# Optimization experiments

Hardware: AMD Instinct MI355X
Metric: run time of the kernel (lower is better)

The kernel has to match this reference:

```python
import jax, jax.numpy as jnp
import numpy as np

KSIZE = 21
PAD = (KSIZE - 1) // 2
SCALE = 4
W0, W1, W2 = 1.0, 1.0, 1.0  # cfg.SOLVER.SR_LOSS_FUNC_SR_WEIGHT


def setup_inputs() -> dict:
    key = jax.random.key(0)
    ks = jax.random.split(key, 7)
    B, C, H, W = 16, 3, 512, 512
    return {
        "hr_pred": jax.random.normal(ks[0], (B, C, H, W), jnp.float32),
        "hr_target": jax.random.normal(ks[1], (B, C, H, W), jnp.float32),
        "lr_target": jax.random.normal(ks[2], (B, C, H // SCALE, W // SCALE), jnp.float32),
        "kernel_pred": jax.random.uniform(ks[3], (B, KSIZE * KSIZE, 64, 64), jnp.float32),
        "gt_kernel": jax.random.uniform(ks[4], (B, 1, KSIZE, KSIZE), jnp.float32),
        "segment_preds": jax.random.uniform(ks[5], (B, 1, H, W), jnp.float32),
        "segment_targets": jax.random.uniform(ks[6], (B, 1, H, W), jnp.float32),
        "iter": 1000,
    }


def _per_sample_blur(img, ker):
    # img: [C,H,W], ker: [k,k] -> depthwise conv with the same kernel on each channel
    C = img.shape[0]
    w = jnp.broadcast_to(ker[None, None], (C, 1, KSIZE, KSIZE))
    out = jax.lax.conv_general_dilated(
        img[None], w, window_strides=(1, 1),
        padding=[(PAD, PAD), (PAD, PAD)], feature_group_count=C)
    return out[0]


def _get_pseudo_lr(sr, kernel_feat):
    # GAP over spatial dims, normalize over channel dim -> per-sample blur kernel
    k = kernel_feat.mean(axis=(2, 3))                      # [B, k*k]
    k = k / k.sum(axis=1, keepdims=True)
    weight = k.reshape(k.shape[0], 1, KSIZE, KSIZE)        # [B,1,k,k]
    blurred = jax.vmap(_per_sample_blur)(sr, weight[:, 0])  # [B,C,H,W]
    B, C, H, W = blurred.shape
    lrs = jax.image.resize(blurred, (B, C, H // SCALE, W // SCALE), method="bicubic")
    return lrs, weight


def reference(hr_pred, hr_target, lr_target, kernel_pred, gt_kernel,
              segment_preds, segment_targets, iter):
    hr_loss = jnp.abs(hr_pred - hr_target)                 # L1, reduction='none'
    lr_pred, kernel_w = _get_pseudo_lr(hr_pred, kernel_pred)
    lr_loss = jnp.abs(lr_pred - lr_target)
    kernel_loss = jnp.square(kernel_w - gt_kernel)         # MSE, reduction='none'
    # ORIENTED_WEIGHT_ITER == -1 -> no crack/seg-fail weighting
    # ONLY_KERNEL_LOSS_FOR_PRETRAIN == False -> full weighted sum
    loss = (W0 * hr_loss.mean(axis=(1, 2, 3))
            + W1 * lr_loss.mean(axis=(1, 2, 3))
            + W2 * kernel_loss.mean(axis=(1, 2, 3)))       # [B]
    return loss, kernel_w
```

## Files before the change

kernel.cpp:

```cpp
#include <hip/hip_runtime.h>

#define NB 16
#define NC 3
#define NH 512
#define NW 512
#define TAPS 441
#define HL 128
#define WL 128

#define WS_KSUM   0
#define WS_WEIGHT 7056
#define WS_FCLASS 14112
#define WS_FPOLY  532512
#define WS_KLMEAN 560160
#define WS_HRPART 560176
#define WS_LRPOLY 561200
#define WS_LREDGE 561968
#define WS_TOTAL  574064
#define WS_LRB    574064
#define WS_W4     577000
#define WS_FPOLY2 3722728
#define WS_TOTAL3 3745256
#define WS_HRP2   3745256
#define WS_TOTAL4 3748328

__device__ inline float keysCubic(float x) {
  if (x < 1.f) return ((1.5f * x - 2.5f) * x) * x + 1.f;
  if (x < 2.f) return ((-0.5f * x + 2.5f) * x - 4.f) * x + 2.f;
  return 0.f;
}

__device__ inline float blockSumAll(float v, volatile float* red, int nw) {
  #pragma unroll
  for (int o = 32; o > 0; o >>= 1) v += __shfl_down(v, o, 64);
  int w = threadIdx.x >> 6, lane = threadIdx.x & 63;
  __syncthreads();
  if (lane == 0) red[w] = v;
  __syncthreads();
  float s = 0.f;
  for (int i = 0; i < nw; i++) s += red[i];
  return s;
}

__global__ void zero_accum(float* p, int n) {
  int t = blockIdx.x * blockDim.x + threadIdx.x;
  if (t < n) p[t] = 0.f;
}

__global__ void kmean_kernel(const float4* __restrict__ kp4, float* __restrict__ ksum) {
  __shared__ float red[4];
  int blk = blockIdx.x;
  int t = threadIdx.x;
  const float4* base = kp4 + (size_t)blk * 1024;
  float s = 0.f;
  #pragma unroll
  for (int i = 0; i < 4; i++) {
    float4 v = base[i * 256 + t];
    s += v.x + v.y + v.z + v.w;
  }
  float tot = blockSumAll(s, red, 4);
  if (t == 0) ksum[blk] = tot * (1.f / 4096.f);
}

__global__ void knorm_kernel(const float* __restrict__ ksum, const float* __restrict__ gt,
                             float* __restrict__ weight, float* __restrict__ kw_out,
                             float* __restrict__ kl_mean) {
  __shared__ float red[8];
  int b = blockIdx.x, t = threadIdx.x;
  float v = (t < TAPS) ? ksum[b * TAPS + t] : 0.f;
  float tot = blockSumAll(v, red, 8);
  float sq = 0.f;
  if (t < TAPS) {
    float w = v / tot;
    weight[b * TAPS + t] = w;
    kw_out[b * TAPS + t] = w;
    float d = w - gt[b * TAPS + t];
    sq = d * d;
  }
  float sqs = blockSumAll(sq, red, 8);
  if (t == 0) kl_mean[b] = sqs * (1.f / (float)TAPS);
}

__global__ void hrloss_kernel(const float4* __restrict__ a, const float4* __restrict__ bb,
                              float* __restrict__ hr_part) {
  __shared__ float red[4];
  int blk = blockIdx.x, t = threadIdx.x;
  int samp = blk >> 6, chunk = blk & 63;
  size_t base = (size_t)samp * 196608 + (size_t)chunk * 3072;
  float s = 0.f;
  #pragma unroll
  for (int i = 0; i < 12; i++) {
    float4 x = a[base + i * 256 + t];
    float4 y = bb[base + i * 256 + t];
    s += fabsf(x.x - y.x) + fabsf(x.y - y.y) + fabsf(x.z - y.z) + fabsf(x.w - y.w);
  }
  float tot = blockSumAll(s, red, 4);
  if (t == 0) hr_part[blk] = tot;
}

__global__ void precls_kernel(const float* __restrict__ ws_weight, float* __restrict__ fclass,
                              float* __restrict__ fpoly, float* __restrict__ fpoly2) {
  __shared__ float ker[441];
  __shared__ float H[21][36];
  __shared__ float Qy[16], Qx[16];
  int cy = blockIdx.x / 5, cx = blockIdx.x % 5, b = blockIdx.y;
  int t = threadIdx.x;
  for (int i = t; i < 441; i += 256) ker[i] = ws_weight[b * 441 + i];
  if (t == 0) {
    const int lo[5] = {6, 2, 0, 0, 0};
    const int hi[5] = {16, 16, 16, 14, 10};
    float s = 0.f;
    for (int k = 0; k < 16; k++) {
      float q = (k >= lo[cy] && k < hi[cy]) ? keysCubic(fabsf((float)k - 7.5f) * 0.25f) : 0.f;
      Qy[k] = q; s += q;
    }
    for (int k = 0; k < 16; k++) Qy[k] /= s;
    s = 0.f;
    for (int k = 0; k < 16; k++) {
      float q = (k >= lo[cx] && k < hi[cx]) ? keysCubic(fabsf((float)k - 7.5f) * 0.25f) : 0.f;
      Qx[k] = q; s += q;
    }
    for (int k = 0; k < 16; k++) Qx[k] /= s;
  }
  bool interior = (cy == 2 && cx == 2);
  if (interior) {
    for (int i = t; i < 1728; i += 256) fpoly[b * 1728 + i] = 0.f;
  }
  __syncthreads();
  for (int i = t; i < 756; i += 256) {
    int ty = i / 36, q = i - (i / 36) * 36;
    float s = 0.f;
    int tx0 = max(0, q - 15), tx1 = min(21, q + 1);
    for (int tx = tx0; tx < tx1; tx++) s += ker[ty * 21 + tx] * Qx[q - tx];
    H[ty][q] = s;
  }
  __syncthreads();
  float* Fb = fclass + ((size_t)b * 25 + (size_t)blockIdx.x) * 1296;
  for (int i = t; i < 1296; i += 256) {
    int p = i / 36, q = i - (i / 36) * 36;
    float s = 0.f;
    int ty0 = max(0, p - 15), ty1 = min(21, p + 1);
    for (int ty = ty0; ty < ty1; ty++) s += Qy[p - ty] * H[ty][q];
    Fb[i] = s;
    if (interior) {
      int phase = (p & 3) * 4 + (q & 3);
      fpoly[b * 1728 + phase * 108 + (p >> 2) * 12 + (q >> 2)] = s;
      if (fpoly2)
        fpoly2[b * 1408 + phase * 88 + (p >> 2) * 9 + (q >> 2)] = s;
    }
  }
}

__global__ __launch_bounds__(256, 5) void conv_phase4f(const float* __restrict__ img,
                                                       const float* __restrict__ tgt,
                                                       const float* __restrict__ fpoly2,
                                                       float* __restrict__ W4,
                                                       float* __restrict__ hrp) {
  __shared__ __align__(16) float SM[7040];
  __shared__ float redh[4];
  int z = blockIdx.z;
  int bc = z >> 2, phy = z & 3;
  int b = bc / 3;
  int tileX = blockIdx.x, tileY = blockIdx.y;
  int t = threadIdx.x;
  int phx = t >> 6;
  int pos = t & 63;
  int gy_ = pos >> 3;
  int gx_ = pos & 7;

  int rowBase = 128 * tileY - 16 + phy;
  int colBase = 128 * tileX - 16;
  const float* imgbc = img + (size_t)bc * (NH * NW);
  const float* tgtbc = tgt + (size_t)bc * (NH * NW);
  float l1 = 0.f;
  for (int idx = t; idx < 1600; idx += 256) {
    int yy = idx / 40, xx = idx - (idx / 40) * 40;
    int gy = rowBase + 4 * yy;
    int gx = colBase + 4 * xx;
    float4 v = {0.f, 0.f, 0.f, 0.f};
    if ((unsigned)gy < (unsigned)NH && (unsigned)gx < (unsigned)NW)
      v = *(const float4*)&imgbc[(size_t)gy * NW + gx];
    SM[0 * 1760 + yy * 44 + xx] = v.x;
    SM[1 * 1760 + yy * 44 + xx] = v.y;
    SM[2 * 1760 + yy * 44 + xx] = v.z;
    SM[3 * 1760 + yy * 44 + xx] = v.w;
    if (yy >= 4 && yy < 36 && xx >= 4 && xx < 36) {
      float4 tv = *(const float4*)&tgtbc[(size_t)gy * NW + gx];
      l1 += fabsf(v.x - tv.x) + fabsf(v.y - tv.y) + fabsf(v.z - tv.z) + fabsf(v.w - tv.w);
    }
  }
  __syncthreads();
  float hsum = blockSumAll(l1, redh, 4);
  if (t == 0) hrp[(blockIdx.z * 4 + blockIdx.y) * 4 + blockIdx.x] = hsum;

  float acc[4][4];
  #pragma unroll
  for (int r = 0; r < 4; r++)
    #pragma unroll
    for (int j = 0; j < 4; j++) acc[r][j] = 0.f;

  int foff = __builtin_amdgcn_readfirstlane(b * 1408 + (phy * 4 + phx) * 88);
  const float* fk = fpoly2 + foff;
  int smbase = __builtin_amdgcn_readfirstlane(phx * 1760);
  const float* Sp = &SM[smbase];
  #pragma unroll
  for (int m = 0; m < 12; m++) {
    const float* srow = &Sp[(4 * gy_ + m) * 44 + 4 * gx_];
    float4 a0 = *(const float4*)srow;
    float4 a1 = *(const float4*)(srow + 4);
    float4 a2 = *(const float4*)(srow + 8);
    float rowv[12] = {a0.x, a0.y, a0.z, a0.w, a1.x, a1.y, a1.z, a1.w,
                      a2.x, a2.y, a2.z, a2.w};
    #pragma unroll
    for (int r = 0; r < 4; r++) {
      int uy = m - r;
      if (uy >= 0 && uy < 9) {
        #pragma unroll
        for (int q = 0; q < 9; q++) {
          float fv = fk[uy * 9 + q];
          #pragma unroll
          for (int j = 0; j < 4; j++)
            acc[r][j] = fmaf(fv, rowv[q + j], acc[r][j]);
        }
      }
    }
  }

  __syncthreads();
  #pragma unroll
  for (int r = 0; r < 4; r++) {
    float4 s = {acc[r][0], acc[r][1], acc[r][2], acc[r][3]};
    *(float4*)&SM[phx * 1024 + (4 * gy_ + r) * 32 + 4 * gx_] = s;
  }
  __syncthreads();

  const float4* R0 = (const float4*)&SM[0];
  const float4* R1 = (const float4*)&SM[1024];
  const float4* R2 = (const float4*)&SM[2048];
  const float4* R3 = (const float4*)&SM[3072];
  float4 v0 = R0[t], v1 = R1[t], v2 = R2[t], v3 = R3[t];
  float4 s;
  s.x = v0.x + v1.x + v2.x + v3.x;
  s.y = v0.y + v1.y + v2.y + v3.y;
  s.z = v0.z + v1.z + v2.z + v3.z;
  s.w = v0.w + v1.w + v2.w + v3.w;

  int oy = 32 * tileY + (t >> 3);
  int ox = 32 * tileX + 4 * (t & 7);
  float* dst = W4 + ((size_t)phy * 48 + bc) * (HL * WL) + (size_t)oy * WL + ox;
  *(float4*)dst = s;
}

__global__ __launch_bounds__(256) void lrsum_kernel(const float* __restrict__ W4,
                                                    const float* __restrict__ lr_tgt,
                                                    float* __restrict__ lr_b) {
  __shared__ float red[4];
  int bc = blockIdx.y;
  int idx = blockIdx.x * 256 + threadIdx.x;
  float l = 0.f;
  if (idx < 15376) {
    int oy = 2 + idx / 124;
    int ox = 2 + (idx - (idx / 124) * 124);
    size_t base = (size_t)bc * (HL * WL) + (size_t)oy * WL + ox;
    const size_t PL = (size_t)48 * HL * WL;
    float s = W4[base] + W4[base + PL] + W4[base + 2 * PL] + W4[base + 3 * PL];
    l = fabsf(s - lr_tgt[base]);
  }
  float tot = blockSumAll(l, red, 4);
  if (threadIdx.x == 0) lr_b[bc * 61 + blockIdx.x] = tot;
}

__global__ __launch_bounds__(128) void fused_poly(const float* __restrict__ img,
                                                  const float* __restrict__ lr_tgt,
                                                  const float4* __restrict__ fpoly4,
                                                  float* __restrict__ lr_poly) {
  __shared__ __align__(16) float S[4][40][44];
  __shared__ float red[2];
  int tileX = blockIdx.x, tileY = blockIdx.y, bc = blockIdx.z;
  int b = bc / 3;
  int t = threadIdx.x;
  int oyT = t >> 2, oxG = t & 3;
  const float* imgbc = img + (size_t)bc * (NH * NW);
  const float4* fp4 = fpoly4 + b * 432;
  float acc[8] = {0.f, 0.f, 0.f, 0.f, 0.f, 0.f, 0.f, 0.f};
  int rowBase = 128 * tileY - 16;
  int colBase = 128 * tileX - 16;
  for (int phy = 0; phy < 4; phy++) {
    for (int idx = t; idx < 1600; idx += 128) {
      int yy = idx / 40, xx = idx - yy * 40;
      int gy = rowBase + 4 * yy + phy;
      int gx = colBase + 4 * xx;
      float4 v = {0.f, 0.f, 0.f, 0.f};
      if ((unsigned)gy < (unsigned)NH && (unsigned)gx < (unsigned)NW)
        v = *(const float4*)&imgbc[(size_t)gy * NW + gx];
      S[0][yy][xx] = v.x; S[1][yy][xx] = v.y; S[2][yy][xx] = v.z; S[3][yy][xx] = v.w;
    }
    __syncthreads();
    #pragma unroll
    for (int phx = 0; phx < 4; phx++) {
      const float4* fprow = fp4 + (phy * 4 + phx) * 27;
      for (int uy = 0; uy < 9; uy++) {
        const float* srow = &S[phx][oyT + uy][oxG * 8];
        float4 w0 = *(const float4*)(srow);
        float4 w1 = *(const float4*)(srow + 4);
        float4 w2 = *(const float4*)(srow + 8);
        float4 w3 = *(const float4*)(srow + 12);
        float w[16] = {w0.x, w0.y, w0.z, w0.w, w1.x, w1.y, w1.z, w1.w,
                       w2.x, w2.y, w2.z, w2.w, w3.x, w3.y, w3.z, w3.w};
        float4 f0 = fprow[uy * 3], f1 = fprow[uy * 3 + 1], f2 = fprow[uy * 3 + 2];
        float f[9] = {f0.x, f0.y, f0.z, f0.w, f1.x, f1.y, f1.z, f1.w, f2.x};
        #pragma unroll
        for (int q = 0; q < 9; q++) {
          #pragma unroll
          for (int r = 0; r < 8; r++) acc[r] = fmaf(f[q], w[q + r], acc[r]);
        }
      }
    }
    __syncthreads();
  }
  int oy = 32 * tileY + oyT;
  float l = 0.f;
  if (oy >= 2 && oy < 126) {
    const float* tg = lr_tgt + (size_t)bc * (HL * WL) + (size_t)oy * WL + 32 * tileX + oxG * 8;
    #pragma unroll
    for (int r = 0; r < 8; r++) {
      int ox = 32 * tileX + oxG * 8 + r;
      if (ox >= 2 && ox < 126) l += fabsf(acc[r] - tg[r]);
    }
  }
  float tot = blockSumAll(l, red, 2);
  if (t == 0) lr_poly[bc * 16 + tileY * 4 + tileX] = tot;
}

__global__ __launch_bounds__(256) void edge_kernel(const float* __restrict__ img,
                                                   const float* __restrict__ lr_tgt,
                                                   const float* __restrict__ fclass,
                                                   float* __restrict__ lr_edge) {
  __shared__ float red[4];
  int bc = blockIdx.y, b = bc / 3;
  int wid = threadIdx.x >> 6, lane = threadIdx.x & 63;
  int idx = blockIdx.x * 4 + wid;
  int oy, ox;
  if (idx < 512) {
    int e = idx >> 7;
    oy = (e < 2) ? e : (124 + e);
    ox = idx & 127;
  } else {
    int j = idx - 512;
    oy = 2 + (j >> 2);
    int c = j & 3;
    ox = (c < 2) ? c : (124 + c);
  }
  int cy = (oy == 0) ? 0 : (oy == 1) ? 1 : (oy == 126) ? 3 : (oy == 127) ? 4 : 2;
  int cx = (ox == 0) ? 0 : (ox == 1) ? 1 : (ox == 126) ? 3 : (ox == 127) ? 4 : 2;
  const float* F = fclass + ((size_t)b * 25 + (size_t)(cy * 5 + cx)) * 1296;
  const float* imgbc = img + (size_t)bc * (NH * NW);
  int gy0 = 4 * oy - 16, gx0 = 4 * ox - 16;
  float acc = 0.f;
  #pragma unroll 3
  for (int tp = lane; tp < 1296; tp += 64) {
    int p = (unsigned)tp / 36u;
    int q = tp - p * 36;
    int gy = gy0 + p, gx = gx0 + q;
    float v = 0.f;
    if ((unsigned)gy < (unsigned)NH && (unsigned)gx < (unsigned)NW)
      v = imgbc[gy * NW + gx];
    acc = fmaf(F[tp], v, acc);
  }
  #pragma unroll
  for (int o = 32; o > 0; o >>= 1) acc += __shfl_down(acc, o, 64);
  __syncthreads();
  if (lane == 0) {
    float tgt = lr_tgt[(size_t)bc * (HL * WL) + (size_t)oy * WL + ox];
    red[wid] = fabsf(acc - tgt);
  }
  __syncthreads();
  if (threadIdx.x == 0) {
    lr_edge[bc * 252 + blockIdx.x] = red[0] + red[1] + red[2] + red[3];
  }
}

__global__ void final_big4(const float* __restrict__ hrp, const float* __restrict__ lr_b,
                           const float* __restrict__ lr_edge, const float* __restrict__ kl_mean,
                           float* __restrict__ out) {
  __shared__ float red[4];
  int b = blockIdx.x, t = threadIdx.x;
  float hs = 0.f;
  for (int i = t; i < 192; i += 256) hs += hrp[b * 192 + i];
  float h = blockSumAll(hs, red, 4);
  float ls = 0.f;
  for (int i = t; i < 183; i += 256) ls += lr_b[b * 183 + i];
  for (int i = t; i < 756; i += 256) ls += lr_edge[b * 756 + i];
  float l = blockSumAll(ls, red, 4);
  if (t == 0)
    out[b] = h * (1.f / 786432.f) + l * (1.f / 49152.f) + kl_mean[b];
}

__global__ void final_reduce(const float* __restrict__ hr_part, const float* __restrict__ lr_poly,
                             const float* __restrict__ lr_edge, const float* __restrict__ kl_mean,
                             float* __restrict__ out) {
  __shared__ float red[4];
  int b = blockIdx.x, t = threadIdx.x;
  float hs = 0.f;
  for (int i = t; i < 64; i += 256) hs += hr_part[b * 64 + i];
  float h = blockSumAll(hs, red, 4);
  float ls = 0.f;
  for (int i = t; i < 48; i += 256) ls += lr_poly[b * 48 + i];
  for (int i = t; i < 756; i += 256) ls += lr_edge[b * 756 + i];
  float l = blockSumAll(ls, red, 4);
  if (t == 0)
    out[b] = h * (1.f / 786432.f) + l * (1.f / 49152.f) + kl_mean[b];
}

extern "C" void kernel_launch(void* const* d_in, const int* in_sizes, int n_in,
                              void* d_out, int out_size, void* d_ws, size_t ws_size,
                              hipStream_t stream) {
  const float* hr_pred = (const float*)d_in[0];
  const float* hr_target = (const float*)d_in[1];
  const float* lr_target = (const float*)d_in[2];
  const float* kernel_pred = (const float*)d_in[3];
  const float* gt_kernel = (const float*)d_in[4];
  float* out = (float*)d_out;
  float* ws = (float*)d_ws;

  bool big4 = ws_size >= (size_t)WS_TOTAL4 * sizeof(float);
  bool big = ws_size >= (size_t)WS_TOTAL * sizeof(float);
  float* ksum = ws + WS_KSUM;
  float* weight = ws + WS_WEIGHT;

  if (big) {
    float* fclass = ws + WS_FCLASS;
    float* fpoly = ws + WS_FPOLY;
    float* kl_mean = ws + WS_KLMEAN;
    float* lr_edge = ws + WS_LREDGE;
    float* fpoly2 = big4 ? (ws + WS_FPOLY2) : nullptr;
    kmean_kernel<<<NB * TAPS, 256, 0, stream>>>((const float4*)kernel_pred, ksum);
    knorm_kernel<<<NB, 512, 0, stream>>>(ksum, gt_kernel, weight, out + NB, kl_mean);
    precls_kernel<<<dim3(25, NB), 256, 0, stream>>>(weight, fclass, fpoly, fpoly2);
    edge_kernel<<<dim3(252, NB * NC), 256, 0, stream>>>(hr_pred, lr_target, fclass, lr_edge);
    if (big4) {
      float* lr_b = ws + WS_LRB;
      float* W4 = ws + WS_W4;
      float* hrp = ws + WS_HRP2;
      conv_phase4f<<<dim3(4, 4, NB * NC * 4), 256, 0, stream>>>(hr_pred, hr_target, fpoly2,
                                                                W4, hrp);
      lrsum_kernel<<<dim3(61, NB * NC), 256, 0, stream>>>(W4, lr_target, lr_b);
      final_big4<<<NB, 256, 0, stream>>>(hrp, lr_b, lr_edge, kl_mean, out);
    } else {
      float* hr_part = ws + WS_HRPART;
      float* lr_poly = ws + WS_LRPOLY;
      hrloss_kernel<<<NB * 64, 256, 0, stream>>>((const float4*)hr_pred,
                                                 (const float4*)hr_target, hr_part);
      fused_poly<<<dim3(4, 4, NB * NC), 128, 0, stream>>>(hr_pred, lr_target,
                                                          (const float4*)fpoly, lr_poly);
      final_reduce<<<NB, 256, 0, stream>>>(hr_part, lr_poly, lr_edge, kl_mean, out);
    }
  } else {
    float* hr_sum = ws + 14112;
    float* lr_sum = hr_sum + 16;
    float* kl_mean = hr_sum + 32;
    zero_accum<<<1, 64, 0, stream>>>(hr_sum, 48);
    kmean_kernel<<<NB * TAPS, 256, 0, stream>>>((const float4*)kernel_pred, ksum);
    knorm_kernel<<<NB, 512, 0, stream>>>(ksum, gt_kernel, weight, out + NB, kl_mean);
    hrloss_kernel<<<NB * 64, 256, 0, stream>>>((const float4*)hr_pred, (const float4*)hr_target,
                                               ksum);
    final_reduce<<<NB, 256, 0, stream>>>(ksum, lr_sum, lr_sum, kl_mean, out);
  }
}
```

Measured before the change: 124.1 us.

## Merge edge-pixel kernel into main conv kernel via interleaved block ranges

Folds the separate edge_kernel launch into the phase-conv kernel. A 1D grid of 79*192 blocks is split so each group of 79 runs 16 interior conv blocks and 63 border-pixel blocks. This removes one launch and the serialization between the edge and conv stages, so the light edge work can overlap with the heavy conv blocks. In exchange, the merged kernel carries the larger launch bounds and shared memory footprint for the edge blocks, and blockIdx is decoded by hand.

After: 128.2 us. +3.4%, slower.

```diff
diff --git a/kernel.cpp b/kernel.cpp
--- a/kernel.cpp
+++ b/kernel.cpp
@@ -20,7 +20,6 @@
 #define WS_LRB    574064
 #define WS_W4     577000
 #define WS_FPOLY2 3722728
-#define WS_TOTAL3 3745256
 #define WS_HRP2   3745256
 #define WS_TOTAL4 3748328
 
@@ -151,18 +150,70 @@
   }
 }
 
-__global__ __launch_bounds__(256, 5) void conv_phase4f(const float* __restrict__ img,
-                                                       const float* __restrict__ tgt,
-                                                       const float* __restrict__ fpoly2,
-                                                       float* __restrict__ W4,
-                                                       float* __restrict__ hrp) {
+__global__ __launch_bounds__(256, 5) void main_fused(const float* __restrict__ img,
+                                                     const float* __restrict__ tgt,
+                                                     const float* __restrict__ lr_tgt,
+                                                     const float* __restrict__ fpoly2,
+                                                     const float* __restrict__ fclass,
+                                                     float* __restrict__ W4,
+                                                     float* __restrict__ hrp,
+                                                     float* __restrict__ lr_edge) {
   __shared__ __align__(16) float SM[7040];
   __shared__ float redh[4];
-  int z = blockIdx.z;
+  int bid = blockIdx.x;
+  int g = bid / 79, r = bid - g * 79;
+  int t = threadIdx.x;
+
+  if (r >= 16) {
+    int eb = g * 63 + (r - 16);
+    int bc = eb / 252, xblk = eb - bc * 252;
+    int b = bc / 3;
+    int wid = t >> 6, lane = t & 63;
+    int idx = xblk * 4 + wid;
+    int oy, ox;
+    if (idx < 512) {
+      int e = idx >> 7;
+      oy = (e < 2) ? e : (124 + e);
+      ox = idx & 127;
+    } else {
+      int j = idx - 512;
+      oy = 2 + (j >> 2);
+      int c = j & 3;
+      ox = (c < 2) ? c : (124 + c);
+    }
+    int cy = (oy == 0) ? 0 : (oy == 1) ? 1 : (oy == 126) ? 3 : (oy == 127) ? 4 : 2;
+    int cx = (ox == 0) ? 0 : (ox == 1) ? 1 : (ox == 126) ? 3 : (ox == 127) ? 4 : 2;
+    const float* F = fclass + ((size_t)b * 25 + (size_t)(cy * 5 + cx)) * 1296;
+    const float* imgbc = img + (size_t)bc * (NH * NW);
+    int gy0 = 4 * oy - 16, gx0 = 4 * ox - 16;
+    float acc = 0.f;
+    #pragma unroll 3
+    for (int tp = lane; tp < 1296; tp += 64) {
+      int p = (unsigned)tp / 36u;
+      int q = tp - p * 36;
+      int gy = gy0 + p, gx = gx0 + q;
+      float v = 0.f;
+      if ((unsigned)gy < (unsigned)NH && (unsigned)gx < (unsigned)NW)
+        v = imgbc[gy * NW + gx];
+      acc = fmaf(F[tp], v, acc);
+    }
+    #pragma unroll
+    for (int o = 32; o > 0; o >>= 1) acc += __shfl_down(acc, o, 64);
+    __syncthreads();
+    if (lane == 0) {
+      float tv = lr_tgt[(size_t)bc * (HL * WL) + (size_t)oy * WL + ox];
+      redh[wid] = fabsf(acc - tv);
+    }
+    __syncthreads();
+    if (t == 0)
+      lr_edge[bc * 252 + xblk] = redh[0] + redh[1] + redh[2] + redh[3];
+    return;
+  }
+
+  int cb = g * 16 + r;
+  int tileX = cb & 3, tileY = (cb >> 2) & 3, z = cb >> 4;
   int bc = z >> 2, phy = z & 3;
   int b = bc / 3;
-  int tileX = blockIdx.x, tileY = blockIdx.y;
-  int t = threadIdx.x;
   int phx = t >> 6;
   int pos = t & 63;
   int gy_ = pos >> 3;
@@ -191,13 +242,13 @@
   }
   __syncthreads();
   float hsum = blockSumAll(l1, redh, 4);
-  if (t == 0) hrp[(blockIdx.z * 4 + blockIdx.y) * 4 + blockIdx.x] = hsum;
+  if (t == 0) hrp[(z * 4 + tileY) * 4 + tileX] = hsum;
 
   float acc[4][4];
   #pragma unroll
-  for (int r = 0; r < 4; r++)
+  for (int rr = 0; rr < 4; rr++)
     #pragma unroll
-    for (int j = 0; j < 4; j++) acc[r][j] = 0.f;
+    for (int j = 0; j < 4; j++) acc[rr][j] = 0.f;
 
   int foff = __builtin_amdgcn_readfirstlane(b * 1408 + (phy * 4 + phx) * 88);
   const float* fk = fpoly2 + foff;
@@ -212,15 +263,15 @@
     float rowv[12] = {a0.x, a0.y, a0.z, a0.w, a1.x, a1.y, a1.z, a1.w,
                       a2.x, a2.y, a2.z, a2.w};
     #pragma unroll
-    for (int r = 0; r < 4; r++) {
-      int uy = m - r;
+    for (int rr = 0; rr < 4; rr++) {
+      int uy = m - rr;
       if (uy >= 0 && uy < 9) {
         #pragma unroll
         for (int q = 0; q < 9; q++) {
           float fv = fk[uy * 9 + q];
           #pragma unroll
           for (int j = 0; j < 4; j++)
-            acc[r][j] = fmaf(fv, rowv[q + j], acc[r][j]);
+            acc[rr][j] = fmaf(fv, rowv[q + j], acc[rr][j]);
         }
       }
     }
@@ -228,9 +279,9 @@
 
   __syncthreads();
   #pragma unroll
-  for (int r = 0; r < 4; r++) {
-    float4 s = {acc[r][0], acc[r][1], acc[r][2], acc[r][3]};
-    *(float4*)&SM[phx * 1024 + (4 * gy_ + r) * 32 + 4 * gx_] = s;
+  for (int rr = 0; rr < 4; rr++) {
+    float4 s = {acc[rr][0], acc[rr][1], acc[rr][2], acc[rr][3]};
+    *(float4*)&SM[phx * 1024 + (4 * gy_ + rr) * 32 + 4 * gx_] = s;
   }
   __syncthreads();
 
@@ -437,13 +488,12 @@
     kmean_kernel<<<NB * TAPS, 256, 0, stream>>>((const float4*)kernel_pred, ksum);
     knorm_kernel<<<NB, 512, 0, stream>>>(ksum, gt_kernel, weight, out + NB, kl_mean);
     precls_kernel<<<dim3(25, NB), 256, 0, stream>>>(weight, fclass, fpoly, fpoly2);
-    edge_kernel<<<dim3(252, NB * NC), 256, 0, stream>>>(hr_pred, lr_target, fclass, lr_edge);
     if (big4) {
       float* lr_b = ws + WS_LRB;
       float* W4 = ws + WS_W4;
       float* hrp = ws + WS_HRP2;
-      conv_phase4f<<<dim3(4, 4, NB * NC * 4), 256, 0, stream>>>(hr_pred, hr_target, fpoly2,
-                                                                W4, hrp);
+      main_fused<<<79 * 192, 256, 0, stream>>>(hr_pred, hr_target, lr_target, fpoly2, fclass,
+                                               W4, hrp, lr_edge);
       lrsum_kernel<<<dim3(61, NB * NC), 256, 0, stream>>>(W4, lr_target, lr_b);
       final_big4<<<NB, 256, 0, stream>>>(hrp, lr_b, lr_edge, kl_mean, out);
     } else {
@@ -451,6 +501,7 @@
       float* lr_poly = ws + WS_LRPOLY;
       hrloss_kernel<<<NB * 64, 256, 0, stream>>>((const float4*)hr_pred,
                                                  (const float4*)hr_target, hr_part);
+      edge_kernel<<<dim3(252, NB * NC), 256, 0, stream>>>(hr_pred, lr_target, fclass, lr_edge);
       fused_poly<<<dim3(4, 4, NB * NC), 128, 0, stream>>>(hr_pred, lr_target,
                                                           (const float4*)fpoly, lr_poly);
       final_reduce<<<NB, 256, 0, stream>>>(hr_part, lr_poly, lr_edge, kl_mean, out);
```
